# Kernel optimization log

Measured on AMD Instinct MI355X. Metric: run time of the kernel, lower is better.

The kernel has to match this reference:

```python
import jax, jax.numpy as jnp
import numpy as np

N_NODES = 50000
N_EDGES = 800000
D_FEAT = 64
N_CLASSES = 40


def setup_inputs() -> dict:
    key = jax.random.key(0)
    ks = jax.random.split(key, 8)
    x = jax.random.normal(ks[0], (N_NODES, D_FEAT), dtype=jnp.float32)
    edge_index = jax.random.randint(ks[1], (2, N_EDGES), 0, N_NODES, dtype=jnp.int64)
    # GCNConv weights (glorot-ish scale) and post-aggregation biases
    s1 = 1.0 / np.sqrt(D_FEAT)
    W1 = jax.random.normal(ks[2], (D_FEAT, D_FEAT), dtype=jnp.float32) * s1
    b1 = jnp.zeros((D_FEAT,), dtype=jnp.float32)
    W2 = jax.random.normal(ks[3], (D_FEAT, D_FEAT), dtype=jnp.float32) * s1
    b2 = jnp.zeros((D_FEAT,), dtype=jnp.float32)
    W3 = jax.random.normal(ks[4], (D_FEAT, N_CLASSES), dtype=jnp.float32) * s1
    b3 = jnp.zeros((N_CLASSES,), dtype=jnp.float32)
    return {"x": x, "edge_index": edge_index, "W1": W1, "b1": b1,
            "W2": W2, "b2": b2, "W3": W3, "b3": b3}


def _gcn_layer(x, src, dst, norm, W, b, n_nodes):
    # dense transform then normalized neighbor aggregation (PyG GCNConv)
    h = x @ W                                   # [N, out]
    msgs = h[src] * norm[:, None]               # gather over edges [E+N, out]
    agg = jax.ops.segment_sum(msgs, dst, num_segments=n_nodes)
    return agg + b


def reference(x, edge_index, W1, b1, W2, b2, W3, b3):
    n = x.shape[0]
    loops = jnp.arange(n, dtype=edge_index.dtype)
    src = jnp.concatenate([edge_index[0], loops])   # add self-loops
    dst = jnp.concatenate([edge_index[1], loops])
    # symmetric normalization: deg over targets incl. self-loops
    deg = jax.ops.segment_sum(jnp.ones_like(dst, dtype=x.dtype), dst, num_segments=n)
    dinv = jnp.where(deg > 0, jax.lax.rsqrt(deg), 0.0)
    norm = dinv[src] * dinv[dst]                    # [E+N]
    for W, b in ((W1, b1), (W2, b2), (W3, b3)):
        x = jax.nn.relu(_gcn_layer(x, src, dst, norm, W, b, n))
        # dropout treated as identity (deterministic eval reference)
    return jax.nn.log_softmax(x, axis=-1)
```

## Files before the change

### kernel.cpp

```cpp
#include <hip/hip_runtime.h>
#include <math.h>


#define DF 64
#define TB 256
#define NPART 8

typedef __attribute__((ext_vector_type(8))) short bf16x8;
typedef __attribute__((ext_vector_type(4))) float f32x4;

__device__ __forceinline__ unsigned short f2bf(float f) {
    union { float f; unsigned u; } c; c.f = f;
    unsigned u = c.u;
    return (unsigned short)((u + 0x7fffu + ((u >> 16) & 1u)) >> 16);
}
__device__ __forceinline__ float bf2f(unsigned short h) {
    union { unsigned u; float f; } c; c.u = ((unsigned)h) << 16;
    return c.f;
}
__device__ __forceinline__ void acc_bf16x8(uint4 v, float* a) {
    a[0] += bf2f((unsigned short)(v.x & 0xffffu));
    a[1] += bf2f((unsigned short)(v.x >> 16));
    a[2] += bf2f((unsigned short)(v.y & 0xffffu));
    a[3] += bf2f((unsigned short)(v.y >> 16));
    a[4] += bf2f((unsigned short)(v.z & 0xffffu));
    a[5] += bf2f((unsigned short)(v.z >> 16));
    a[6] += bf2f((unsigned short)(v.w & 0xffffu));
    a[7] += bf2f((unsigned short)(v.w >> 16));
}
__device__ __forceinline__ void acc_bf16x4(uint2 v, float* a) {
    a[0] += bf2f((unsigned short)(v.x & 0xffffu));
    a[1] += bf2f((unsigned short)(v.x >> 16));
    a[2] += bf2f((unsigned short)(v.y & 0xffffu));
    a[3] += bf2f((unsigned short)(v.y >> 16));
}

__global__ void zero_int_kernel(int* __restrict__ p, int n) {
    int i = blockIdx.x * blockDim.x + threadIdx.x;
    if (i < n) p[i] = 0;
}

__global__ void count_deg_part_kernel(const int* __restrict__ dst, int* __restrict__ deg,
                                      int e, int psize) {
    const int p   = blockIdx.x & (NPART - 1);
    const int sl  = blockIdx.x / NPART;
    const int nsl = gridDim.x / NPART;
    const int lo = p * psize, hi = lo + psize;
    for (int i = sl * TB + threadIdx.x; i < e; i += nsl * TB) {
        int d = dst[i];
        if (d >= lo && d < hi) atomicAdd(&deg[d], 1);
    }
}

__global__ void scan_block_kernel(const int* __restrict__ deg, int* __restrict__ ex,
                                  int* __restrict__ bsum, float* __restrict__ dinv, int n) {
    __shared__ int s[TB];
    const int t = threadIdx.x;
    const int i = blockIdx.x * TB + t;
    int v = (i < n) ? deg[i] : 0;
    if (i < n) dinv[i] = rsqrtf((float)(v + 1));
    s[t] = v; __syncthreads();
#pragma unroll
    for (int o = 1; o < TB; o <<= 1) {
        int u = (t >= o) ? s[t - o] : 0;
        __syncthreads();
        s[t] += u;
        __syncthreads();
    }
    if (i < n) ex[i] = s[t] - v;
    if (t == TB - 1) bsum[blockIdx.x] = s[TB - 1];
}

__global__ void add_offsets_kernel(int* __restrict__ ex, const int* __restrict__ bsum,
                                   int* __restrict__ cursor, int n, int nb) {
    __shared__ int s[TB];
    const int t = threadIdx.x;
    int v = (t < nb) ? bsum[t] : 0;
    s[t] = v; __syncthreads();
#pragma unroll
    for (int o = 1; o < TB; o <<= 1) {
        int u = (t >= o) ? s[t - o] : 0;
        __syncthreads();
        s[t] += u;
        __syncthreads();
    }
    const int boff = (blockIdx.x > 0) ? s[blockIdx.x - 1] : 0;
    const int i = blockIdx.x * TB + t;
    if (i < n) {
        int r = ex[i] + boff;
        ex[i] = r;
        cursor[i] = r;
    }
}

__global__ void fill_csr_part_kernel(const int* __restrict__ src, const int* __restrict__ dst,
                                     int* __restrict__ cursor,
                                     unsigned short* __restrict__ cidx, int e, int psize) {
    const int p   = blockIdx.x & (NPART - 1);
    const int sl  = blockIdx.x / NPART;
    const int nsl = gridDim.x / NPART;
    const int lo = p * psize, hi = lo + psize;
    for (int i = sl * TB + threadIdx.x; i < e; i += nsl * TB) {
        int d = dst[i];
        if (d >= lo && d < hi) {
            int pos = atomicAdd(&cursor[d], 1);
            cidx[pos] = (unsigned short)src[i];
        }
    }
}

template <int NCO, typename TIN>
__global__ __launch_bounds__(256) void gemm_mfma_kernel(
        const TIN* __restrict__ X, const float* __restrict__ W,
        const float* __restrict__ dinv, unsigned short* __restrict__ G, int M) {
    constexpr int NCT = (NCO + 15) / 16;
    const int lane = threadIdx.x & 63;
    const int wid  = threadIdx.x >> 6;
    const int t    = blockIdx.x * 4 + wid;
    const int nt   = (M + 15) >> 4;
    if (t >= nt) return;
    const int n = lane & 15;
    const int g = lane >> 4;

    bf16x8 bf[NCT][2];
#pragma unroll
    for (int ct = 0; ct < NCT; ++ct) {
        const int c = ct * 16 + n;
#pragma unroll
        for (int ks = 0; ks < 2; ++ks) {
#pragma unroll
            for (int j = 0; j < 8; ++j) {
                const int k = ks * 32 + g * 8 + j;
                float w = (c < NCO) ? W[k * NCO + c] : 0.f;
                bf[ct][ks][j] = (short)f2bf(w);
            }
        }
    }

    const int row_a = t * 16 + n;
    const int ra = (row_a < M) ? row_a : (M - 1);
    bf16x8 af[2];
    if (sizeof(TIN) == 4) {
        const float* Xf = (const float*)X;
#pragma unroll
        for (int ks = 0; ks < 2; ++ks) {
            float4 p0 = *(const float4*)(Xf + (size_t)ra * 64 + ks * 32 + g * 8);
            float4 p1 = *(const float4*)(Xf + (size_t)ra * 64 + ks * 32 + g * 8 + 4);
            af[ks][0] = (short)f2bf(p0.x); af[ks][1] = (short)f2bf(p0.y);
            af[ks][2] = (short)f2bf(p0.z); af[ks][3] = (short)f2bf(p0.w);
            af[ks][4] = (short)f2bf(p1.x); af[ks][5] = (short)f2bf(p1.y);
            af[ks][6] = (short)f2bf(p1.z); af[ks][7] = (short)f2bf(p1.w);
        }
    } else {
        const short* Xh = (const short*)X;
#pragma unroll
        for (int ks = 0; ks < 2; ++ks)
            af[ks] = *(const bf16x8*)(Xh + (size_t)ra * 64 + ks * 32 + g * 8);
    }

    const int rbase = t * 16 + g * 4;
    float di[4];
#pragma unroll
    for (int r = 0; r < 4; ++r) {
        int rr = rbase + r;
        di[r] = dinv[(rr < M) ? rr : (M - 1)];
    }

#pragma unroll
    for (int ct = 0; ct < NCT; ++ct) {
        f32x4 acc = {0.f, 0.f, 0.f, 0.f};
        acc = __builtin_amdgcn_mfma_f32_16x16x32_bf16(af[0], bf[ct][0], acc, 0, 0, 0);
        acc = __builtin_amdgcn_mfma_f32_16x16x32_bf16(af[1], bf[ct][1], acc, 0, 0, 0);
        const int col = ct * 16 + n;
#pragma unroll
        for (int r = 0; r < 4; ++r) {
            const int row = rbase + r;
            if (row < M && col < NCO)
                G[(size_t)row * NCO + col] = f2bf(acc[r] * di[r]);
        }
    }
}

__global__ void agg64_kernel(const unsigned short* __restrict__ G,
                             const int* __restrict__ rowptr, const int* __restrict__ deg,
                             const unsigned short* __restrict__ cidx,
                             const float* __restrict__ dinv, const float* __restrict__ b,
                             unsigned short* __restrict__ Y, int M) {
    const int lane = threadIdx.x & 63;
    const int node = blockIdx.x * 4 + (threadIdx.x >> 6);
    if (node >= M) return;
    const int grp = lane >> 3;
    const int sub = lane & 7;
    const int start = rowptr[node];
    const int cnt = deg[node];

    float a[8] = {0.f, 0.f, 0.f, 0.f, 0.f, 0.f, 0.f, 0.f};
    float c[8] = {0.f, 0.f, 0.f, 0.f, 0.f, 0.f, 0.f, 0.f};

    for (int base = 0; base < cnt; base += 64) {
        const int nthis = min(64, cnt - base);
        int myidx = (lane < nthis) ? (int)cidx[start + base + lane] : 0;
        int j = 0;
        for (; j + 16 <= nthis; j += 16) {
            int s0 = __shfl(myidx, j + grp, 64);
            int s1 = __shfl(myidx, j + 8 + grp, 64);
            uint4 v0 = *(const uint4*)(G + (size_t)s0 * 64 + sub * 8);
            uint4 v1 = *(const uint4*)(G + (size_t)s1 * 64 + sub * 8);
            acc_bf16x8(v0, a);
            acc_bf16x8(v1, c);
        }
        if (j + 8 <= nthis) {
            int s0 = __shfl(myidx, j + grp, 64);
            uint4 v0 = *(const uint4*)(G + (size_t)s0 * 64 + sub * 8);
            acc_bf16x8(v0, a);
            j += 8;
        }
        const int rem = nthis - j;
        if (grp < rem) {
            int s0 = __shfl(myidx, j + grp, 64);
            uint4 v0 = *(const uint4*)(G + (size_t)s0 * 64 + sub * 8);
            acc_bf16x8(v0, c);
        }
    }
#pragma unroll
    for (int k = 0; k < 8; ++k) a[k] += c[k];
#pragma unroll
    for (int k = 0; k < 8; ++k) {
        a[k] += __shfl_xor(a[k], 8, 64);
        a[k] += __shfl_xor(a[k], 16, 64);
        a[k] += __shfl_xor(a[k], 32, 64);
    }
    if (grp != 0) return;
    uint4 sv = *(const uint4*)(G + (size_t)node * 64 + sub * 8);
    float self[8];
    self[0] = bf2f((unsigned short)(sv.x & 0xffffu)); self[1] = bf2f((unsigned short)(sv.x >> 16));
    self[2] = bf2f((unsigned short)(sv.y & 0xffffu)); self[3] = bf2f((unsigned short)(sv.y >> 16));
    self[4] = bf2f((unsigned short)(sv.z & 0xffffu)); self[5] = bf2f((unsigned short)(sv.z >> 16));
    self[6] = bf2f((unsigned short)(sv.w & 0xffffu)); self[7] = bf2f((unsigned short)(sv.w >> 16));
    float4 b0 = *(const float4*)(b + sub * 8);
    float4 b1 = *(const float4*)(b + sub * 8 + 4);
    const float di = dinv[node];
    float v[8];
    v[0] = fmaxf((a[0] + self[0]) * di + b0.x, 0.f);
    v[1] = fmaxf((a[1] + self[1]) * di + b0.y, 0.f);
    v[2] = fmaxf((a[2] + self[2]) * di + b0.z, 0.f);
    v[3] = fmaxf((a[3] + self[3]) * di + b0.w, 0.f);
    v[4] = fmaxf((a[4] + self[4]) * di + b1.x, 0.f);
    v[5] = fmaxf((a[5] + self[5]) * di + b1.y, 0.f);
    v[6] = fmaxf((a[6] + self[6]) * di + b1.z, 0.f);
    v[7] = fmaxf((a[7] + self[7]) * di + b1.w, 0.f);
    uint4 o;
    o.x = (unsigned)f2bf(v[0]) | ((unsigned)f2bf(v[1]) << 16);
    o.y = (unsigned)f2bf(v[2]) | ((unsigned)f2bf(v[3]) << 16);
    o.z = (unsigned)f2bf(v[4]) | ((unsigned)f2bf(v[5]) << 16);
    o.w = (unsigned)f2bf(v[6]) | ((unsigned)f2bf(v[7]) << 16);
    *((uint4*)(Y + (size_t)node * 64 + sub * 8)) = o;
}

__global__ void agg40_lsm_kernel(const unsigned short* __restrict__ G,
                                 const int* __restrict__ rowptr, const int* __restrict__ deg,
                                 const unsigned short* __restrict__ cidx,
                                 const float* __restrict__ dinv, const float* __restrict__ b,
                                 float* __restrict__ Y, int M) {
    constexpr int NC = 40;
    constexpr int NQ = 10;
    const int lane = threadIdx.x & 63;
    const int node = blockIdx.x * 4 + (threadIdx.x >> 6);
    if (node >= M) return;
    const int grp = lane >> 4;
    const int sub = lane & 15;
    const bool act = (sub < NQ);
    const int start = rowptr[node];
    const int cnt = deg[node];

    float a[4] = {0.f, 0.f, 0.f, 0.f};
    float c[4] = {0.f, 0.f, 0.f, 0.f};

    for (int base = 0; base < cnt; base += 64) {
        const int nthis = min(64, cnt - base);
        int myidx = (lane < nthis) ? (int)cidx[start + base + lane] : 0;
        int j = 0;
        for (; j + 8 <= nthis; j += 8) {
            int s0 = __shfl(myidx, j + grp, 64);
            int s1 = __shfl(myidx, j + 4 + grp, 64);
            if (act) {
                uint2 v0 = *(const uint2*)(G + (size_t)s0 * NC + sub * 4);
                uint2 v1 = *(const uint2*)(G + (size_t)s1 * NC + sub * 4);
                acc_bf16x4(v0, a);
                acc_bf16x4(v1, c);
            }
        }
        if (j + 4 <= nthis) {
            int s0 = __shfl(myidx, j + grp, 64);
            if (act) {
                uint2 v0 = *(const uint2*)(G + (size_t)s0 * NC + sub * 4);
                acc_bf16x4(v0, a);
            }
            j += 4;
        }
        const int rem = nthis - j;
        if (grp < rem) {
            int s0 = __shfl(myidx, j + grp, 64);
            if (act) {
                uint2 v0 = *(const uint2*)(G + (size_t)s0 * NC + sub * 4);
                acc_bf16x4(v0, c);
            }
        }
    }
#pragma unroll
    for (int k = 0; k < 4; ++k) a[k] += c[k];
#pragma unroll
    for (int k = 0; k < 4; ++k) {
        a[k] += __shfl_xor(a[k], 16, 64);
        a[k] += __shfl_xor(a[k], 32, 64);
    }
    float v[4];
    {
        float self[4] = {0.f, 0.f, 0.f, 0.f};
        float4 bb = make_float4(0.f, 0.f, 0.f, 0.f);
        if (act) {
            uint2 sv = *(const uint2*)(G + (size_t)node * NC + sub * 4);
            self[0] = bf2f((unsigned short)(sv.x & 0xffffu));
            self[1] = bf2f((unsigned short)(sv.x >> 16));
            self[2] = bf2f((unsigned short)(sv.y & 0xffffu));
            self[3] = bf2f((unsigned short)(sv.y >> 16));
            bb = *(const float4*)(b + sub * 4);
        }
        const float di = dinv[node];
        v[0] = fmaxf((a[0] + self[0]) * di + bb.x, 0.f);
        v[1] = fmaxf((a[1] + self[1]) * di + bb.y, 0.f);
        v[2] = fmaxf((a[2] + self[2]) * di + bb.z, 0.f);
        v[3] = fmaxf((a[3] + self[3]) * di + bb.w, 0.f);
    }
    float m = act ? fmaxf(fmaxf(v[0], v[1]), fmaxf(v[2], v[3])) : -INFINITY;
#pragma unroll
    for (int o = 1; o < 16; o <<= 1) m = fmaxf(m, __shfl_xor(m, o, 64));
    float es = act ? (expf(v[0] - m) + expf(v[1] - m) + expf(v[2] - m) + expf(v[3] - m)) : 0.f;
#pragma unroll
    for (int o = 1; o < 16; o <<= 1) es += __shfl_xor(es, o, 64);
    const float ls = logf(es);
    if (act && grp == 0) {
        *((float4*)(Y + (size_t)node * NC + sub * 4)) =
            make_float4(v[0] - m - ls, v[1] - m - ls, v[2] - m - ls, v[3] - m - ls);
    }
}

extern "C" void kernel_launch(void* const* d_in, const int* in_sizes, int n_in,
                              void* d_out, int out_size, void* d_ws, size_t ws_size,
                              hipStream_t stream) {
    const float* x  = (const float*)d_in[0];
    const int*   ei = (const int*)d_in[1];
    const float* W1 = (const float*)d_in[2];
    const float* b1 = (const float*)d_in[3];
    const float* W2 = (const float*)d_in[4];
    const float* b2 = (const float*)d_in[5];
    const float* W3 = (const float*)d_in[6];
    const float* b3 = (const float*)d_in[7];
    float* out = (float*)d_out;

    const int M  = in_sizes[0] / DF;
    const int E  = in_sizes[1] / 2;
    (void)ws_size; (void)n_in; (void)out_size;

    const int* src = ei;
    const int* dst = ei + E;

    const size_t Ma = ((size_t)M + 63) & ~63ull;
    const size_t Ea = ((size_t)E + 63) & ~63ull;

    int* deg    = (int*)d_ws;
    int* rowptr = deg + Ma;
    int* cursor = rowptr + Ma;
    int* bsum   = cursor + Ma;
    unsigned short* cidx = (unsigned short*)(bsum + 256);
    float* dinv = (float*)(cidx + Ea);
    unsigned short* G0 = (unsigned short*)(dinv + Ma);
    unsigned short* G1 = G0 + Ma * DF;

    const int gN = (M + TB - 1) / TB;
    const int nb = gN;
    const int psize = (M + NPART - 1) / NPART;
    const int partGrd = NPART * 96;

    zero_int_kernel<<<gN, TB, 0, stream>>>(deg, M);
    count_deg_part_kernel<<<partGrd, TB, 0, stream>>>(dst, deg, E, psize);
    scan_block_kernel<<<nb, TB, 0, stream>>>(deg, rowptr, bsum, dinv, M);
    add_offsets_kernel<<<nb, TB, 0, stream>>>(rowptr, bsum, cursor, M, nb);
    fill_csr_part_kernel<<<partGrd, TB, 0, stream>>>(src, dst, cursor, cidx, E, psize);

    const int nt      = (M + 15) / 16;
    const int gemmGrd = (nt + 3) / 4;
    const int aggGrd  = (M + 3) / 4;

    gemm_mfma_kernel<64, float><<<gemmGrd, TB, 0, stream>>>(x, W1, dinv, G0, M);
    agg64_kernel<<<aggGrd, TB, 0, stream>>>(G0, rowptr, deg, cidx, dinv, b1, G1, M);
    gemm_mfma_kernel<64, unsigned short><<<gemmGrd, TB, 0, stream>>>(G1, W2, dinv, G0, M);
    agg64_kernel<<<aggGrd, TB, 0, stream>>>(G0, rowptr, deg, cidx, dinv, b2, G1, M);
    gemm_mfma_kernel<40, unsigned short><<<gemmGrd, TB, 0, stream>>>(G1, W3, dinv, G0, M);
    agg40_lsm_kernel<<<aggGrd, TB, 0, stream>>>(G0, rowptr, deg, cidx, dinv, b3, out, M);
}
```

Baseline: 196.4 us.

## Fuse neighbor aggregation with next layer's MFMA transform via shared memory

Layers 1 and 2's aggregation is merged with the next layer's dense transform in one kernel. Each block aggregates 16 nodes into a bf16 tile in LDS, then runs an MFMA against the next weight matrix. This removes two kernel launches and the global write and read of the intermediate activations. In exchange, each block reloads and converts the weights, waves wait at a barrier, and there are 16 nodes per block instead of 4, which may cut latency hiding for the irregular gathers.

```diff
diff --git a/kernel.cpp b/kernel.cpp
--- a/kernel.cpp
+++ b/kernel.cpp
@@ -109,11 +109,9 @@
     }
 }
 
-template <int NCO, typename TIN>
 __global__ __launch_bounds__(256) void gemm_mfma_kernel(
-        const TIN* __restrict__ X, const float* __restrict__ W,
+        const float* __restrict__ X, const float* __restrict__ W,
         const float* __restrict__ dinv, unsigned short* __restrict__ G, int M) {
-    constexpr int NCT = (NCO + 15) / 16;
     const int lane = threadIdx.x & 63;
     const int wid  = threadIdx.x >> 6;
     const int t    = blockIdx.x * 4 + wid;
@@ -122,40 +120,28 @@
     const int n = lane & 15;
     const int g = lane >> 4;
 
-    bf16x8 bf[NCT][2];
-#pragma unroll
-    for (int ct = 0; ct < NCT; ++ct) {
+    bf16x8 bf[4][2];
+#pragma unroll
+    for (int ct = 0; ct < 4; ++ct) {
         const int c = ct * 16 + n;
 #pragma unroll
-        for (int ks = 0; ks < 2; ++ks) {
-#pragma unroll
-            for (int j = 0; j < 8; ++j) {
-                const int k = ks * 32 + g * 8 + j;
-                float w = (c < NCO) ? W[k * NCO + c] : 0.f;
-                bf[ct][ks][j] = (short)f2bf(w);
-            }
-        }
+        for (int ks = 0; ks < 2; ++ks)
+#pragma unroll
+            for (int j = 0; j < 8; ++j)
+                bf[ct][ks][j] = (short)f2bf(W[(ks * 32 + g * 8 + j) * 64 + c]);
     }
 
     const int row_a = t * 16 + n;
     const int ra = (row_a < M) ? row_a : (M - 1);
     bf16x8 af[2];
-    if (sizeof(TIN) == 4) {
-        const float* Xf = (const float*)X;
-#pragma unroll
-        for (int ks = 0; ks < 2; ++ks) {
-            float4 p0 = *(const float4*)(Xf + (size_t)ra * 64 + ks * 32 + g * 8);
-            float4 p1 = *(const float4*)(Xf + (size_t)ra * 64 + ks * 32 + g * 8 + 4);
-            af[ks][0] = (short)f2bf(p0.x); af[ks][1] = (short)f2bf(p0.y);
-            af[ks][2] = (short)f2bf(p0.z); af[ks][3] = (short)f2bf(p0.w);
-            af[ks][4] = (short)f2bf(p1.x); af[ks][5] = (short)f2bf(p1.y);
-            af[ks][6] = (short)f2bf(p1.z); af[ks][7] = (short)f2bf(p1.w);
-        }
-    } else {
-        const short* Xh = (const short*)X;
-#pragma unroll
-        for (int ks = 0; ks < 2; ++ks)
-            af[ks] = *(const bf16x8*)(Xh + (size_t)ra * 64 + ks * 32 + g * 8);
+#pragma unroll
+    for (int ks = 0; ks < 2; ++ks) {
+        float4 p0 = *(const float4*)(X + (size_t)ra * 64 + ks * 32 + g * 8);
+        float4 p1 = *(const float4*)(X + (size_t)ra * 64 + ks * 32 + g * 8 + 4);
+        af[ks][0] = (short)f2bf(p0.x); af[ks][1] = (short)f2bf(p0.y);
+        af[ks][2] = (short)f2bf(p0.z); af[ks][3] = (short)f2bf(p0.w);
+        af[ks][4] = (short)f2bf(p1.x); af[ks][5] = (short)f2bf(p1.y);
+        af[ks][6] = (short)f2bf(p1.z); af[ks][7] = (short)f2bf(p1.w);
     }
 
     const int rbase = t * 16 + g * 4;
@@ -167,7 +153,7 @@
     }
 
 #pragma unroll
-    for (int ct = 0; ct < NCT; ++ct) {
+    for (int ct = 0; ct < 4; ++ct) {
         f32x4 acc = {0.f, 0.f, 0.f, 0.f};
         acc = __builtin_amdgcn_mfma_f32_16x16x32_bf16(af[0], bf[ct][0], acc, 0, 0, 0);
         acc = __builtin_amdgcn_mfma_f32_16x16x32_bf16(af[1], bf[ct][1], acc, 0, 0, 0);
@@ -175,86 +161,127 @@
 #pragma unroll
         for (int r = 0; r < 4; ++r) {
             const int row = rbase + r;
-            if (row < M && col < NCO)
-                G[(size_t)row * NCO + col] = f2bf(acc[r] * di[r]);
-        }
-    }
-}
-
-__global__ void agg64_kernel(const unsigned short* __restrict__ G,
-                             const int* __restrict__ rowptr, const int* __restrict__ deg,
-                             const unsigned short* __restrict__ cidx,
-                             const float* __restrict__ dinv, const float* __restrict__ b,
-                             unsigned short* __restrict__ Y, int M) {
-    const int lane = threadIdx.x & 63;
-    const int node = blockIdx.x * 4 + (threadIdx.x >> 6);
-    if (node >= M) return;
+            if (row < M)
+                G[(size_t)row * 64 + col] = f2bf(acc[r] * di[r]);
+        }
+    }
+}
+
+template <int NCO>
+__global__ __launch_bounds__(256) void aggmm_kernel(
+        const unsigned short* __restrict__ G,
+        const int* __restrict__ rowptr, const int* __restrict__ deg,
+        const unsigned short* __restrict__ cidx,
+        const float* __restrict__ dinv, const float* __restrict__ b,
+        const float* __restrict__ Wn,
+        unsigned short* __restrict__ Gout, int M) {
+    __shared__ unsigned short Ys[16][72];
+    __shared__ float ds[16];
+    const int tid  = threadIdx.x;
+    const int lane = tid & 63;
+    const int wid  = tid >> 6;
+    const int base = blockIdx.x * 16;
     const int grp = lane >> 3;
     const int sub = lane & 7;
-    const int start = rowptr[node];
-    const int cnt = deg[node];
-
-    float a[8] = {0.f, 0.f, 0.f, 0.f, 0.f, 0.f, 0.f, 0.f};
-    float c[8] = {0.f, 0.f, 0.f, 0.f, 0.f, 0.f, 0.f, 0.f};
-
-    for (int base = 0; base < cnt; base += 64) {
-        const int nthis = min(64, cnt - base);
-        int myidx = (lane < nthis) ? (int)cidx[start + base + lane] : 0;
-        int j = 0;
-        for (; j + 16 <= nthis; j += 16) {
-            int s0 = __shfl(myidx, j + grp, 64);
-            int s1 = __shfl(myidx, j + 8 + grp, 64);
-            uint4 v0 = *(const uint4*)(G + (size_t)s0 * 64 + sub * 8);
-            uint4 v1 = *(const uint4*)(G + (size_t)s1 * 64 + sub * 8);
-            acc_bf16x8(v0, a);
-            acc_bf16x8(v1, c);
-        }
-        if (j + 8 <= nthis) {
-            int s0 = __shfl(myidx, j + grp, 64);
-            uint4 v0 = *(const uint4*)(G + (size_t)s0 * 64 + sub * 8);
-            acc_bf16x8(v0, a);
-            j += 8;
-        }
-        const int rem = nthis - j;
-        if (grp < rem) {
-            int s0 = __shfl(myidx, j + grp, 64);
-            uint4 v0 = *(const uint4*)(G + (size_t)s0 * 64 + sub * 8);
-            acc_bf16x8(v0, c);
-        }
-    }
-#pragma unroll
-    for (int k = 0; k < 8; ++k) a[k] += c[k];
-#pragma unroll
-    for (int k = 0; k < 8; ++k) {
-        a[k] += __shfl_xor(a[k], 8, 64);
-        a[k] += __shfl_xor(a[k], 16, 64);
-        a[k] += __shfl_xor(a[k], 32, 64);
-    }
-    if (grp != 0) return;
-    uint4 sv = *(const uint4*)(G + (size_t)node * 64 + sub * 8);
-    float self[8];
-    self[0] = bf2f((unsigned short)(sv.x & 0xffffu)); self[1] = bf2f((unsigned short)(sv.x >> 16));
-    self[2] = bf2f((unsigned short)(sv.y & 0xffffu)); self[3] = bf2f((unsigned short)(sv.y >> 16));
-    self[4] = bf2f((unsigned short)(sv.z & 0xffffu)); self[5] = bf2f((unsigned short)(sv.z >> 16));
-    self[6] = bf2f((unsigned short)(sv.w & 0xffffu)); self[7] = bf2f((unsigned short)(sv.w >> 16));
-    float4 b0 = *(const float4*)(b + sub * 8);
-    float4 b1 = *(const float4*)(b + sub * 8 + 4);
-    const float di = dinv[node];
-    float v[8];
-    v[0] = fmaxf((a[0] + self[0]) * di + b0.x, 0.f);
-    v[1] = fmaxf((a[1] + self[1]) * di + b0.y, 0.f);
-    v[2] = fmaxf((a[2] + self[2]) * di + b0.z, 0.f);
-    v[3] = fmaxf((a[3] + self[3]) * di + b0.w, 0.f);
-    v[4] = fmaxf((a[4] + self[4]) * di + b1.x, 0.f);
-    v[5] = fmaxf((a[5] + self[5]) * di + b1.y, 0.f);
-    v[6] = fmaxf((a[6] + self[6]) * di + b1.z, 0.f);
-    v[7] = fmaxf((a[7] + self[7]) * di + b1.w, 0.f);
-    uint4 o;
-    o.x = (unsigned)f2bf(v[0]) | ((unsigned)f2bf(v[1]) << 16);
-    o.y = (unsigned)f2bf(v[2]) | ((unsigned)f2bf(v[3]) << 16);
-    o.z = (unsigned)f2bf(v[4]) | ((unsigned)f2bf(v[5]) << 16);
-    o.w = (unsigned)f2bf(v[6]) | ((unsigned)f2bf(v[7]) << 16);
-    *((uint4*)(Y + (size_t)node * 64 + sub * 8)) = o;
+    const int n16 = lane & 15;
+    const int g16 = lane >> 4;
+
+    const bool wactive = (wid * 16 < NCO);
+    bf16x8 bf[2];
+    if (wactive) {
+        const int c = wid * 16 + n16;
+#pragma unroll
+        for (int ks = 0; ks < 2; ++ks)
+#pragma unroll
+            for (int j = 0; j < 8; ++j) {
+                const int k = ks * 32 + g16 * 8 + j;
+                float w = (c < NCO) ? Wn[k * NCO + c] : 0.f;
+                bf[ks][j] = (short)f2bf(w);
+            }
+    }
+
+    for (int i = 0; i < 4; ++i) {
+        const int nrow  = wid * 4 + i;
+        const int node0 = base + nrow;
+        const int node  = (node0 < M) ? node0 : (M - 1);
+        const int start = rowptr[node];
+        const int cnt   = deg[node];
+
+        float a[8] = {0.f, 0.f, 0.f, 0.f, 0.f, 0.f, 0.f, 0.f};
+        float c8[8] = {0.f, 0.f, 0.f, 0.f, 0.f, 0.f, 0.f, 0.f};
+        for (int bs = 0; bs < cnt; bs += 64) {
+            const int nthis = min(64, cnt - bs);
+            int myidx = (lane < nthis) ? (int)cidx[start + bs + lane] : 0;
+            int j = 0;
+            for (; j + 16 <= nthis; j += 16) {
+                int s0 = __shfl(myidx, j + grp, 64);
+                int s1 = __shfl(myidx, j + 8 + grp, 64);
+                uint4 v0 = *(const uint4*)(G + (size_t)s0 * 64 + sub * 8);
+                uint4 v1 = *(const uint4*)(G + (size_t)s1 * 64 + sub * 8);
+                acc_bf16x8(v0, a);
+                acc_bf16x8(v1, c8);
+            }
+            if (j + 8 <= nthis) {
+                int s0 = __shfl(myidx, j + grp, 64);
+                uint4 v0 = *(const uint4*)(G + (size_t)s0 * 64 + sub * 8);
+                acc_bf16x8(v0, a);
+                j += 8;
+            }
+            const int rem = nthis - j;
+            if (grp < rem) {
+                int s0 = __shfl(myidx, j + grp, 64);
+                uint4 v0 = *(const uint4*)(G + (size_t)s0 * 64 + sub * 8);
+                acc_bf16x8(v0, c8);
+            }
+        }
+#pragma unroll
+        for (int k = 0; k < 8; ++k) a[k] += c8[k];
+#pragma unroll
+        for (int k = 0; k < 8; ++k) {
+            a[k] += __shfl_xor(a[k], 8, 64);
+            a[k] += __shfl_xor(a[k], 16, 64);
+            a[k] += __shfl_xor(a[k], 32, 64);
+        }
+        if (grp == 0) {
+            uint4 sv = *(const uint4*)(G + (size_t)node * 64 + sub * 8);
+            float4 b0 = *(const float4*)(b + sub * 8);
+            float4 b1 = *(const float4*)(b + sub * 8 + 4);
+            const float di = dinv[node];
+            float v[8];
+            v[0] = fmaxf((a[0] + bf2f((unsigned short)(sv.x & 0xffffu))) * di + b0.x, 0.f);
+            v[1] = fmaxf((a[1] + bf2f((unsigned short)(sv.x >> 16)))     * di + b0.y, 0.f);
+            v[2] = fmaxf((a[2] + bf2f((unsigned short)(sv.y & 0xffffu))) * di + b0.z, 0.f);
+            v[3] = fmaxf((a[3] + bf2f((unsigned short)(sv.y >> 16)))     * di + b0.w, 0.f);
+            v[4] = fmaxf((a[4] + bf2f((unsigned short)(sv.z & 0xffffu))) * di + b1.x, 0.f);
+            v[5] = fmaxf((a[5] + bf2f((unsigned short)(sv.z >> 16)))     * di + b1.y, 0.f);
+            v[6] = fmaxf((a[6] + bf2f((unsigned short)(sv.w & 0xffffu))) * di + b1.z, 0.f);
+            v[7] = fmaxf((a[7] + bf2f((unsigned short)(sv.w >> 16)))     * di + b1.w, 0.f);
+            uint4 o;
+            o.x = (unsigned)f2bf(v[0]) | ((unsigned)f2bf(v[1]) << 16);
+            o.y = (unsigned)f2bf(v[2]) | ((unsigned)f2bf(v[3]) << 16);
+            o.z = (unsigned)f2bf(v[4]) | ((unsigned)f2bf(v[5]) << 16);
+            o.w = (unsigned)f2bf(v[6]) | ((unsigned)f2bf(v[7]) << 16);
+            *((uint4*)&Ys[nrow][sub * 8]) = o;
+            if (sub == 0) ds[nrow] = di;
+        }
+    }
+    __syncthreads();
+
+    if (!wactive) return;
+    bf16x8 af[2];
+#pragma unroll
+    for (int ks = 0; ks < 2; ++ks)
+        af[ks] = *(const bf16x8*)&Ys[n16][ks * 32 + g16 * 8];
+    f32x4 acc = {0.f, 0.f, 0.f, 0.f};
+    acc = __builtin_amdgcn_mfma_f32_16x16x32_bf16(af[0], bf[0], acc, 0, 0, 0);
+    acc = __builtin_amdgcn_mfma_f32_16x16x32_bf16(af[1], bf[1], acc, 0, 0, 0);
+    const int col = wid * 16 + n16;
+#pragma unroll
+    for (int r = 0; r < 4; ++r) {
+        const int row = base + g16 * 4 + r;
+        if (row < M && col < NCO)
+            Gout[(size_t)row * NCO + col] = f2bf(acc[r] * ds[g16 * 4 + r]);
+    }
 }
 
 __global__ void agg40_lsm_kernel(const unsigned short* __restrict__ G,
@@ -390,12 +417,11 @@
 
     const int nt      = (M + 15) / 16;
     const int gemmGrd = (nt + 3) / 4;
+    const int fusGrd  = nt;
     const int aggGrd  = (M + 3) / 4;
 
-    gemm_mfma_kernel<64, float><<<gemmGrd, TB, 0, stream>>>(x, W1, dinv, G0, M);
-    agg64_kernel<<<aggGrd, TB, 0, stream>>>(G0, rowptr, deg, cidx, dinv, b1, G1, M);
-    gemm_mfma_kernel<64, unsigned short><<<gemmGrd, TB, 0, stream>>>(G1, W2, dinv, G0, M);
-    agg64_kernel<<<aggGrd, TB, 0, stream>>>(G0, rowptr, deg, cidx, dinv, b2, G1, M);
-    gemm_mfma_kernel<40, unsigned short><<<gemmGrd, TB, 0, stream>>>(G1, W3, dinv, G0, M);
+    gemm_mfma_kernel<<<gemmGrd, TB, 0, stream>>>(x, W1, dinv, G0, M);
+    aggmm_kernel<64><<<fusGrd, TB, 0, stream>>>(G0, rowptr, deg, cidx, dinv, b1, W2, G1, M);
+    aggmm_kernel<40><<<fusGrd, TB, 0, stream>>>(G1, rowptr, deg, cidx, dinv, b2, W3, G0, M);
     agg40_lsm_kernel<<<aggGrd, TB, 0, stream>>>(G0, rowptr, deg, cidx, dinv, b3, out, M);
 }
```

Result: no change. 194.6 us (-0.9%).
